# Kernel tuning notes

Measured on AMD Instinct MI355X. Metric: run time of the kernel, lower is better.

## Reference

```python
import jax, jax.numpy as jnp
import numpy as np

ATTRACTION_W = 1.0
REPULSION_W = 1.0
BETA_POS_W = 1.0
BETA_NEG_W = 0.5
K_INST = 256  # max number of distinct instance ids (slice ids)


def setup_inputs() -> dict:
    key = jax.random.key(0)
    B, N, D, K = 4, 65536, 256, K_INST
    k1, k2, k3 = jax.random.split(key, 3)
    beta = jax.random.normal(k1, (B, N, 1), jnp.float32)
    embed = jax.random.normal(k2, (B, N, D), jnp.float32)
    sid = jax.random.randint(k3, (B, N), -1, K)  # -1 = background
    # force exactly one condensation point per instance: hit i (<K) -> sid=i, is_cp
    sid = sid.at[:, :K].set(jnp.broadcast_to(jnp.arange(K), (B, K)))
    is_cp = jnp.zeros((B, N), bool).at[:, :K].set(True)
    return {"beta": beta, "embed": embed, "slice_id": sid, "is_cp": is_cp}


def _loss_single(beta, emb, sid, cp):
    # beta: (N,) logits, emb: (N,D), sid: (N,) int, cp: (N,) bool
    N = sid.shape[0]
    valid = sid >= 0
    cpv = cp & valid  # condensation points with a valid instance id
    # BCE-with-logits: target 1 -> softplus(-x), target 0 -> softplus(x)
    pos = jnp.sum(jnp.where(cpv, jax.nn.softplus(-beta), 0.0)) / jnp.maximum(cpv.sum(), 1)
    noncp = ~cp
    neg = jnp.sum(jnp.where(noncp, jax.nn.softplus(beta), 0.0)) / jnp.maximum(noncp.sum(), 1)
    beta_loss = BETA_POS_W * pos + BETA_NEG_W * neg

    # first CP hit index per instance (segment-min over CP hits), N = "no CP"
    sid_c = jnp.where(valid, sid, 0)
    idx = jnp.arange(N)
    first_cp = jnp.full((K_INST,), N, jnp.int32).at[sid_c].min(
        jnp.where(cpv, idx, N).astype(jnp.int32))
    has_cp = first_cp < N
    cp_emb = emb[jnp.minimum(first_cp, N - 1)]  # (K, D), garbage where no CP

    # attraction: sum over instances of mean ||emb - inst_cp||^2
    d2 = jnp.sum((emb - cp_emb[sid_c]) ** 2, axis=-1)  # (N,)
    w = valid & has_cp[sid_c]
    seg_sum = jnp.zeros((K_INST,), jnp.float32).at[sid_c].add(jnp.where(w, d2, 0.0))
    seg_cnt = jnp.zeros((K_INST,), jnp.float32).at[sid_c].add(w.astype(jnp.float32))
    attraction = jnp.sum(jnp.where(seg_cnt > 0, seg_sum / jnp.maximum(seg_cnt, 1.0), 0.0))
    attraction = attraction * ATTRACTION_W

    # repulsion: mean exp(-||cp_i - cp_j||^2) over all CP pairs (incl. diagonal)
    pd2 = jnp.sum((cp_emb[:, None, :] - cp_emb[None, :, :]) ** 2, axis=-1)  # (K,K)
    pmask = has_cp[:, None] & has_cp[None, :]
    M = has_cp.sum()
    rep = jnp.sum(jnp.where(pmask, jnp.exp(-pd2), 0.0)) / jnp.maximum(M * M, 1)
    rep = jnp.where(M > 1, rep * REPULSION_W, 0.0)

    loss = beta_loss + attraction + rep
    ok = (valid.sum() > 0) & (cpv.sum() > 0)
    return jnp.where(ok, loss, 0.0), ok


def reference(beta, embed, slice_id, is_cp):
    losses, oks = jax.vmap(_loss_single)(beta.squeeze(-1), embed, slice_id, is_cp)
    cnt = oks.sum()
    return jnp.where(cnt > 0, losses.sum() / jnp.maximum(cnt, 1), 0.0)
```

## Files before the change

### kernel.cpp

```cpp
#include <hip/hip_runtime.h>
#include <math.h>

#define K_INST 256
#define ATTRACTION_W 1.0f
#define REPULSION_W 1.0f
#define BETA_POS_W 1.0f
#define BETA_NEG_W 0.5f

__device__ inline float softplusf(float x) {
    return fmaxf(x, 0.f) + log1pf(expf(-fabsf(x)));
}

__device__ inline float waveReduceSumF(float v) {
    for (int o = 32; o; o >>= 1) v += __shfl_xor(v, o);
    return v;
}
__device__ inline int waveReduceSumI(int v) {
    for (int o = 32; o; o >>= 1) v += __shfl_xor(v, o);
    return v;
}

__global__ void init_kernel(int* first_cp, float* seg_sum, int* seg_cnt,
                            float* pos_sum, float* neg_sum, float* rep_sum,
                            int* cpv_cnt, int* noncp_cnt, int* valid_cnt,
                            int N, int B) {
    int idx = blockIdx.x * blockDim.x + threadIdx.x;
    if (idx < B * K_INST) {
        first_cp[idx] = N;
        seg_sum[idx] = 0.f;
        seg_cnt[idx] = 0;
    }
    if (idx < B) {
        pos_sum[idx] = 0.f; neg_sum[idx] = 0.f; rep_sum[idx] = 0.f;
        cpv_cnt[idx] = 0; noncp_cnt[idx] = 0; valid_cnt[idx] = 0;
    }
}

__global__ void stats_kernel(const float* __restrict__ beta,
                             const int* __restrict__ sid,
                             const int* __restrict__ is_cp,
                             int* first_cp,
                             float* pos_sum, float* neg_sum,
                             int* cpv_cnt, int* noncp_cnt, int* valid_cnt,
                             int N) {
    int b = blockIdx.y;
    int base = (blockIdx.x * blockDim.x + threadIdx.x) * 4;
    const float* betaB = beta + (size_t)b * N;
    const int* sidB = sid + (size_t)b * N;
    const int* cpB = is_cp + (size_t)b * N;

    float pos = 0.f, neg = 0.f;
    int c_cpv = 0, c_non = 0, c_val = 0;

    int4 s4 = *(const int4*)(sidB + base);
    int4 c4 = *(const int4*)(cpB + base);
    float4 x4 = *(const float4*)(betaB + base);
    int ss[4] = {s4.x, s4.y, s4.z, s4.w};
    int cc[4] = {c4.x, c4.y, c4.z, c4.w};
    float xx[4] = {x4.x, x4.y, x4.z, x4.w};
    #pragma unroll
    for (int e = 0; e < 4; ++e) {
        bool valid = ss[e] >= 0;
        bool cpv = cc[e] && valid;
        if (cpv) {
            pos += softplusf(-xx[e]);
            c_cpv++;
            atomicMin(&first_cp[b * K_INST + ss[e]], base + e);
        }
        if (!cc[e]) {
            neg += softplusf(xx[e]);
            c_non++;
        }
        c_val += valid ? 1 : 0;
    }

    __shared__ float sf[2][4];
    __shared__ int si[3][4];
    pos = waveReduceSumF(pos);
    neg = waveReduceSumF(neg);
    c_cpv = waveReduceSumI(c_cpv);
    c_non = waveReduceSumI(c_non);
    c_val = waveReduceSumI(c_val);
    int wave = threadIdx.x >> 6, lane = threadIdx.x & 63;
    if (lane == 0) {
        sf[0][wave] = pos; sf[1][wave] = neg;
        si[0][wave] = c_cpv; si[1][wave] = c_non; si[2][wave] = c_val;
    }
    __syncthreads();
    if (threadIdx.x == 0) {
        float p = sf[0][0] + sf[0][1] + sf[0][2] + sf[0][3];
        float n = sf[1][0] + sf[1][1] + sf[1][2] + sf[1][3];
        int a = si[0][0] + si[0][1] + si[0][2] + si[0][3];
        int c = si[1][0] + si[1][1] + si[1][2] + si[1][3];
        int v = si[2][0] + si[2][1] + si[2][2] + si[2][3];
        if (p != 0.f) atomicAdd(&pos_sum[b], p);
        if (n != 0.f) atomicAdd(&neg_sum[b], n);
        if (a) atomicAdd(&cpv_cnt[b], a);
        if (c) atomicAdd(&noncp_cnt[b], c);
        if (v) atomicAdd(&valid_cnt[b], v);
    }
}

__global__ void gather_kernel(const float* __restrict__ embed,
                              const int* __restrict__ first_cp,
                              float* __restrict__ cp_emb,
                              float* __restrict__ cp_embT, int N) {
    int b = blockIdx.y;
    int k0 = blockIdx.x * 64;
    __shared__ float tile[64][257];
    const float* embB = embed + (size_t)b * N * 256;
    const int* fcB = first_cp + b * K_INST;

    int r = threadIdx.x >> 2;
    int q = threadIdx.x & 3;
    int src = fcB[k0 + r];
    if (src >= N) src = N - 1;
    const float4* srow = (const float4*)(embB + (size_t)src * 256);
    float4* drow = (float4*)(cp_emb + ((size_t)b * K_INST + k0 + r) * 256);
    #pragma unroll
    for (int c = 0; c < 16; ++c) {
        float4 v = srow[q * 16 + c];
        drow[q * 16 + c] = v;
        int col = q * 64 + c * 4;
        tile[r][col + 0] = v.x;
        tile[r][col + 1] = v.y;
        tile[r][col + 2] = v.z;
        tile[r][col + 3] = v.w;
    }
    __syncthreads();
    int kk = threadIdx.x & 63;
    int dg = threadIdx.x >> 6;
    float* T = cp_embT + (size_t)b * K_INST * 256;
    #pragma unroll
    for (int dd = 0; dd < 64; ++dd) {
        int d = dg * 64 + dd;
        T[(size_t)d * 256 + k0 + kk] = tile[kk][d];
    }
}

__global__ void attraction_kernel(const float* __restrict__ embed,
                                  const int* __restrict__ sid,
                                  const int* __restrict__ first_cp,
                                  const float* __restrict__ cp_emb,
                                  float* seg_sum, int* seg_cnt,
                                  int N, int blocks_per_batch) {
    int b = blockIdx.y;
    __shared__ float s_sum[K_INST];
    __shared__ int s_cnt[K_INST];
    for (int k = threadIdx.x; k < K_INST; k += blockDim.x) { s_sum[k] = 0.f; s_cnt[k] = 0; }
    __syncthreads();

    int wave = threadIdx.x >> 6;
    int lane = threadIdx.x & 63;
    int waves_per_batch = blocks_per_batch * 4;
    int wid = blockIdx.x * 4 + wave;
    int stride = waves_per_batch * 8;

    const float* embB = embed + (size_t)b * N * 256;
    const float* cpB  = cp_emb + (size_t)b * K_INST * 256;
    const int* sidB   = sid + (size_t)b * N;
    const int* fcB    = first_cp + b * K_INST;

    for (int i = wid * 8; i < N; i += stride) {
        int4 sa = *(const int4*)(sidB + i);
        int4 sb = *(const int4*)(sidB + i + 4);
        int ss[8] = {sa.x, sa.y, sa.z, sa.w, sb.x, sb.y, sb.z, sb.w};

        float4 e[8];
        #pragma unroll
        for (int j = 0; j < 8; ++j)
            e[j] = *(const float4*)(embB + (size_t)(i + j) * 256 + lane * 4);

        float v[8];
        unsigned act = 0;
        #pragma unroll
        for (int j = 0; j < 8; ++j) {
            v[j] = 0.f;
            int s = ss[j];
            if (s >= 0 && fcB[s] < N) {
                act |= (1u << j);
                float4 c = *(const float4*)(cpB + (size_t)s * 256 + lane * 4);
                float d0 = e[j].x - c.x, d1 = e[j].y - c.y;
                float d2 = e[j].z - c.z, d3 = e[j].w - c.w;
                v[j] = d0 * d0 + d1 * d1 + d2 * d2 + d3 * d3;
            }
        }
        #pragma unroll
        for (int j = 0; j < 8; ++j) v[j] = waveReduceSumF(v[j]);
        if (lane == 0) {
            #pragma unroll
            for (int j = 0; j < 8; ++j) {
                if (act & (1u << j)) {
                    atomicAdd(&s_sum[ss[j]], v[j]);
                    atomicAdd(&s_cnt[ss[j]], 1);
                }
            }
        }
    }
    __syncthreads();
    for (int k = threadIdx.x; k < K_INST; k += blockDim.x) {
        if (s_cnt[k]) {
            atomicAdd(&seg_sum[b * K_INST + k], s_sum[k]);
            atomicAdd(&seg_cnt[b * K_INST + k], s_cnt[k]);
        }
    }
}

__global__ void repulsion_kernel(const float* __restrict__ cp_emb,
                                 const float* __restrict__ cp_embT,
                                 const int* __restrict__ first_cp,
                                 float* rep_sum, int N) {
    int b = blockIdx.y;
    int i0 = blockIdx.x * 8;
    __shared__ float srow[8][260];
    const float* cpB = cp_emb + (size_t)b * K_INST * 256;
    const float* T = cp_embT + (size_t)b * K_INST * 256;

    {
        int r = threadIdx.x >> 5, cc = (threadIdx.x & 31) * 8;
        float4 a = *(const float4*)(cpB + (size_t)(i0 + r) * 256 + cc);
        float4 bv = *(const float4*)(cpB + (size_t)(i0 + r) * 256 + cc + 4);
        srow[r][cc + 0] = a.x;  srow[r][cc + 1] = a.y;
        srow[r][cc + 2] = a.z;  srow[r][cc + 3] = a.w;
        srow[r][cc + 4] = bv.x; srow[r][cc + 5] = bv.y;
        srow[r][cc + 6] = bv.z; srow[r][cc + 7] = bv.w;
    }
    __syncthreads();

    int j = threadIdx.x;
    bool has_j = first_cp[b * K_INST + j] < N;
    float acc[8] = {0.f, 0.f, 0.f, 0.f, 0.f, 0.f, 0.f, 0.f};
    for (int d = 0; d < 256; d += 2) {
        float v0 = T[(size_t)d * 256 + j];
        float v1 = T[(size_t)(d + 1) * 256 + j];
        #pragma unroll
        for (int r = 0; r < 8; ++r) {
            float f0 = srow[r][d] - v0;
            float f1 = srow[r][d + 1] - v1;
            acc[r] += f0 * f0 + f1 * f1;
        }
    }
    float val = 0.f;
    #pragma unroll
    for (int r = 0; r < 8; ++r) {
        bool has_i = first_cp[b * K_INST + i0 + r] < N;
        if (has_i && has_j) val += expf(-acc[r]);
    }
    __shared__ float sf[4];
    val = waveReduceSumF(val);
    int wave = threadIdx.x >> 6, lane = threadIdx.x & 63;
    if (lane == 0) sf[wave] = val;
    __syncthreads();
    if (threadIdx.x == 0) {
        atomicAdd(&rep_sum[b], sf[0] + sf[1] + sf[2] + sf[3]);
    }
}

__global__ void final_kernel(const int* __restrict__ first_cp,
                             const float* __restrict__ seg_sum,
                             const int* __restrict__ seg_cnt,
                             const float* __restrict__ pos_sum,
                             const float* __restrict__ neg_sum,
                             const float* __restrict__ rep_sum,
                             const int* __restrict__ cpv_cnt,
                             const int* __restrict__ noncp_cnt,
                             const int* __restrict__ valid_cnt,
                             float* out, int N, int B) {
    __shared__ float s_att[4];
    __shared__ int s_m[4];
    float loss_sum = 0.f;
    int ok_cnt = 0;
    int wave = threadIdx.x >> 6, lane = threadIdx.x & 63;
    for (int b = 0; b < B; ++b) {
        int k = threadIdx.x;
        int fc = first_cp[b * K_INST + k];
        int has = (fc < N) ? 1 : 0;
        int cnt = seg_cnt[b * K_INST + k];
        float att = (cnt > 0) ? (seg_sum[b * K_INST + k] / (float)cnt) : 0.f;
        att = waveReduceSumF(att);
        has = waveReduceSumI(has);
        if (lane == 0) { s_att[wave] = att; s_m[wave] = has; }
        __syncthreads();
        if (threadIdx.x == 0) {
            float attraction = (s_att[0] + s_att[1] + s_att[2] + s_att[3]) * ATTRACTION_W;
            int M = s_m[0] + s_m[1] + s_m[2] + s_m[3];
            float pos = pos_sum[b] / fmaxf((float)cpv_cnt[b], 1.f);
            float neg = neg_sum[b] / fmaxf((float)noncp_cnt[b], 1.f);
            float beta_loss = BETA_POS_W * pos + BETA_NEG_W * neg;
            float rep = 0.f;
            if (M > 1) {
                float mm = (float)M * (float)M;
                rep = (rep_sum[b] / fmaxf(mm, 1.f)) * REPULSION_W;
            }
            float loss = beta_loss + attraction + rep;
            bool ok = (valid_cnt[b] > 0) && (cpv_cnt[b] > 0);
            if (ok) { loss_sum += loss; ok_cnt += 1; }
        }
        __syncthreads();
    }
    if (threadIdx.x == 0) {
        out[0] = (ok_cnt > 0) ? (loss_sum / (float)ok_cnt) : 0.f;
    }
}

extern "C" void kernel_launch(void* const* d_in, const int* in_sizes, int n_in,
                              void* d_out, int out_size, void* d_ws, size_t ws_size,
                              hipStream_t stream) {
    const float* beta  = (const float*)d_in[0];
    const float* embed = (const float*)d_in[1];
    const int* sid     = (const int*)d_in[2];
    const int* is_cp   = (const int*)d_in[3];
    float* out = (float*)d_out;

    const int N = 65536;
    const int B = in_sizes[0] / N;
    (void)n_in; (void)out_size; (void)ws_size;

    char* ws = (char*)d_ws;
    int*   first_cp  = (int*)(ws + 0);
    float* seg_sum   = (float*)(ws + 4096);
    int*   seg_cnt   = (int*)(ws + 8192);
    float* pos_sum   = (float*)(ws + 12288);
    float* neg_sum   = (float*)(ws + 12352);
    float* rep_sum   = (float*)(ws + 12416);
    int*   cpv_cnt   = (int*)(ws + 12480);
    int*   noncp_cnt = (int*)(ws + 12544);
    int*   valid_cnt = (int*)(ws + 12608);
    float* cp_emb    = (float*)(ws + 16384);
    float* cp_embT   = (float*)(ws + 16384 + (size_t)B * K_INST * 256 * 4);

    init_kernel<<<dim3((B * K_INST + 255) / 256), dim3(256), 0, stream>>>(
        first_cp, seg_sum, seg_cnt, pos_sum, neg_sum, rep_sum,
        cpv_cnt, noncp_cnt, valid_cnt, N, B);

    stats_kernel<<<dim3(N / 1024, B), dim3(256), 0, stream>>>(
        beta, sid, is_cp, first_cp, pos_sum, neg_sum,
        cpv_cnt, noncp_cnt, valid_cnt, N);

    gather_kernel<<<dim3(K_INST / 64, B), dim3(256), 0, stream>>>(
        embed, first_cp, cp_emb, cp_embT, N);

    const int blocks_per_batch = 512;
    attraction_kernel<<<dim3(blocks_per_batch, B), dim3(256), 0, stream>>>(
        embed, sid, first_cp, cp_emb, seg_sum, seg_cnt, N, blocks_per_batch);

    repulsion_kernel<<<dim3(K_INST / 8, B), dim3(256), 0, stream>>>(
        cp_emb, cp_embT, first_cp, rep_sum, N);

    final_kernel<<<dim3(1), dim3(256), 0, stream>>>(
        first_cp, seg_sum, seg_cnt, pos_sum, neg_sum, rep_sum,
        cpv_cnt, noncp_cnt, valid_cnt, out, N, B);
}
```

Before: 120.0 us.

## Fuse attraction and repulsion into one launch and simplify stats and gather

Attraction and repulsion now run in a single kernel: the first 32 blocks per batch compute repulsion and the remaining 512 do the attraction pass, so one launch and its serialization gap go away and the small repulsion work overlaps the bandwidth-bound attraction. The attraction loop now issues all centroid loads without branching, clamping invalid ids to row 0, and applies the validity check only at accumulation time, which gives more memory-level parallelism. The stats kernel processes one element per thread instead of four, with four times as many blocks. The gather kernel uses one 64-thread block per instance and writes the transpose directly, without shared memory. These changes trade vectorised loads and coalesced transpose writes for more parallelism and fewer launches.

```diff
diff --git a/kernel.cpp b/kernel.cpp
--- a/kernel.cpp
+++ b/kernel.cpp
@@ -44,34 +44,24 @@
                              int* cpv_cnt, int* noncp_cnt, int* valid_cnt,
                              int N) {
     int b = blockIdx.y;
-    int base = (blockIdx.x * blockDim.x + threadIdx.x) * 4;
-    const float* betaB = beta + (size_t)b * N;
-    const int* sidB = sid + (size_t)b * N;
-    const int* cpB = is_cp + (size_t)b * N;
-
+    int i = blockIdx.x * blockDim.x + threadIdx.x;
+    size_t gi = (size_t)b * N + i;
+    int s = sid[gi];
+    int cp = is_cp[gi];
+    float x = beta[gi];
+
+    bool valid = s >= 0;
+    bool cpv = cp && valid;
     float pos = 0.f, neg = 0.f;
-    int c_cpv = 0, c_non = 0, c_val = 0;
-
-    int4 s4 = *(const int4*)(sidB + base);
-    int4 c4 = *(const int4*)(cpB + base);
-    float4 x4 = *(const float4*)(betaB + base);
-    int ss[4] = {s4.x, s4.y, s4.z, s4.w};
-    int cc[4] = {c4.x, c4.y, c4.z, c4.w};
-    float xx[4] = {x4.x, x4.y, x4.z, x4.w};
-    #pragma unroll
-    for (int e = 0; e < 4; ++e) {
-        bool valid = ss[e] >= 0;
-        bool cpv = cc[e] && valid;
-        if (cpv) {
-            pos += softplusf(-xx[e]);
-            c_cpv++;
-            atomicMin(&first_cp[b * K_INST + ss[e]], base + e);
-        }
-        if (!cc[e]) {
-            neg += softplusf(xx[e]);
-            c_non++;
-        }
-        c_val += valid ? 1 : 0;
+    int c_cpv = 0, c_non = 0, c_val = valid ? 1 : 0;
+    if (cpv) {
+        pos = softplusf(-x);
+        c_cpv = 1;
+        atomicMin(&first_cp[b * K_INST + s], i);
+    }
+    if (!cp) {
+        neg = softplusf(x);
+        c_non = 1;
     }
 
     __shared__ float sf[2][4];
@@ -106,153 +96,133 @@
                               float* __restrict__ cp_emb,
                               float* __restrict__ cp_embT, int N) {
     int b = blockIdx.y;
-    int k0 = blockIdx.x * 64;
-    __shared__ float tile[64][257];
+    int k = blockIdx.x;
+    int src = first_cp[b * K_INST + k];
+    if (src >= N) src = N - 1;
+    int lane = threadIdx.x;
     const float* embB = embed + (size_t)b * N * 256;
-    const int* fcB = first_cp + b * K_INST;
-
-    int r = threadIdx.x >> 2;
-    int q = threadIdx.x & 3;
-    int src = fcB[k0 + r];
-    if (src >= N) src = N - 1;
-    const float4* srow = (const float4*)(embB + (size_t)src * 256);
-    float4* drow = (float4*)(cp_emb + ((size_t)b * K_INST + k0 + r) * 256);
-    #pragma unroll
-    for (int c = 0; c < 16; ++c) {
-        float4 v = srow[q * 16 + c];
-        drow[q * 16 + c] = v;
-        int col = q * 64 + c * 4;
-        tile[r][col + 0] = v.x;
-        tile[r][col + 1] = v.y;
-        tile[r][col + 2] = v.z;
-        tile[r][col + 3] = v.w;
-    }
-    __syncthreads();
-    int kk = threadIdx.x & 63;
-    int dg = threadIdx.x >> 6;
+    float4 v = ((const float4*)(embB + (size_t)src * 256))[lane];
+    ((float4*)(cp_emb + ((size_t)b * K_INST + k) * 256))[lane] = v;
     float* T = cp_embT + (size_t)b * K_INST * 256;
-    #pragma unroll
-    for (int dd = 0; dd < 64; ++dd) {
-        int d = dg * 64 + dd;
-        T[(size_t)d * 256 + k0 + kk] = tile[kk][d];
-    }
-}
-
-__global__ void attraction_kernel(const float* __restrict__ embed,
-                                  const int* __restrict__ sid,
-                                  const int* __restrict__ first_cp,
-                                  const float* __restrict__ cp_emb,
-                                  float* seg_sum, int* seg_cnt,
-                                  int N, int blocks_per_batch) {
+    int d = lane * 4;
+    T[(size_t)(d + 0) * 256 + k] = v.x;
+    T[(size_t)(d + 1) * 256 + k] = v.y;
+    T[(size_t)(d + 2) * 256 + k] = v.z;
+    T[(size_t)(d + 3) * 256 + k] = v.w;
+}
+
+__global__ void attraction_repulsion_kernel(
+        const float* __restrict__ embed,
+        const int* __restrict__ sid,
+        const int* __restrict__ first_cp,
+        const float* __restrict__ cp_emb,
+        const float* __restrict__ cp_embT,
+        float* seg_sum, int* seg_cnt, float* rep_sum,
+        int N, int atr_blocks) {
     int b = blockIdx.y;
     __shared__ float s_sum[K_INST];
     __shared__ int s_cnt[K_INST];
-    for (int k = threadIdx.x; k < K_INST; k += blockDim.x) { s_sum[k] = 0.f; s_cnt[k] = 0; }
-    __syncthreads();
-
-    int wave = threadIdx.x >> 6;
-    int lane = threadIdx.x & 63;
-    int waves_per_batch = blocks_per_batch * 4;
-    int wid = blockIdx.x * 4 + wave;
-    int stride = waves_per_batch * 8;
-
-    const float* embB = embed + (size_t)b * N * 256;
-    const float* cpB  = cp_emb + (size_t)b * K_INST * 256;
-    const int* sidB   = sid + (size_t)b * N;
-    const int* fcB    = first_cp + b * K_INST;
-
-    for (int i = wid * 8; i < N; i += stride) {
-        int4 sa = *(const int4*)(sidB + i);
-        int4 sb = *(const int4*)(sidB + i + 4);
-        int ss[8] = {sa.x, sa.y, sa.z, sa.w, sb.x, sb.y, sb.z, sb.w};
-
-        float4 e[8];
-        #pragma unroll
-        for (int j = 0; j < 8; ++j)
-            e[j] = *(const float4*)(embB + (size_t)(i + j) * 256 + lane * 4);
-
-        float v[8];
-        unsigned act = 0;
-        #pragma unroll
-        for (int j = 0; j < 8; ++j) {
-            v[j] = 0.f;
-            int s = ss[j];
-            if (s >= 0 && fcB[s] < N) {
-                act |= (1u << j);
-                float4 c = *(const float4*)(cpB + (size_t)s * 256 + lane * 4);
-                float d0 = e[j].x - c.x, d1 = e[j].y - c.y;
-                float d2 = e[j].z - c.z, d3 = e[j].w - c.w;
-                v[j] = d0 * d0 + d1 * d1 + d2 * d2 + d3 * d3;
-            }
-        }
-        #pragma unroll
-        for (int j = 0; j < 8; ++j) v[j] = waveReduceSumF(v[j]);
-        if (lane == 0) {
-            #pragma unroll
-            for (int j = 0; j < 8; ++j) {
-                if (act & (1u << j)) {
-                    atomicAdd(&s_sum[ss[j]], v[j]);
-                    atomicAdd(&s_cnt[ss[j]], 1);
-                }
-            }
-        }
-    }
-    __syncthreads();
-    for (int k = threadIdx.x; k < K_INST; k += blockDim.x) {
-        if (s_cnt[k]) {
-            atomicAdd(&seg_sum[b * K_INST + k], s_sum[k]);
-            atomicAdd(&seg_cnt[b * K_INST + k], s_cnt[k]);
-        }
-    }
-}
-
-__global__ void repulsion_kernel(const float* __restrict__ cp_emb,
-                                 const float* __restrict__ cp_embT,
-                                 const int* __restrict__ first_cp,
-                                 float* rep_sum, int N) {
-    int b = blockIdx.y;
-    int i0 = blockIdx.x * 8;
     __shared__ float srow[8][260];
+    __shared__ float sf[4];
+
     const float* cpB = cp_emb + (size_t)b * K_INST * 256;
-    const float* T = cp_embT + (size_t)b * K_INST * 256;
-
-    {
-        int r = threadIdx.x >> 5, cc = (threadIdx.x & 31) * 8;
-        float4 a = *(const float4*)(cpB + (size_t)(i0 + r) * 256 + cc);
-        float4 bv = *(const float4*)(cpB + (size_t)(i0 + r) * 256 + cc + 4);
-        srow[r][cc + 0] = a.x;  srow[r][cc + 1] = a.y;
-        srow[r][cc + 2] = a.z;  srow[r][cc + 3] = a.w;
-        srow[r][cc + 4] = bv.x; srow[r][cc + 5] = bv.y;
-        srow[r][cc + 6] = bv.z; srow[r][cc + 7] = bv.w;
-    }
-    __syncthreads();
-
-    int j = threadIdx.x;
-    bool has_j = first_cp[b * K_INST + j] < N;
-    float acc[8] = {0.f, 0.f, 0.f, 0.f, 0.f, 0.f, 0.f, 0.f};
-    for (int d = 0; d < 256; d += 2) {
-        float v0 = T[(size_t)d * 256 + j];
-        float v1 = T[(size_t)(d + 1) * 256 + j];
+    const int* fcB = first_cp + b * K_INST;
+
+    if (blockIdx.x < 32) {
+        int i0 = blockIdx.x * 8;
+        const float* T = cp_embT + (size_t)b * K_INST * 256;
+        {
+            int r = threadIdx.x >> 5, cc = (threadIdx.x & 31) * 8;
+            float4 a = *(const float4*)(cpB + (size_t)(i0 + r) * 256 + cc);
+            float4 bv = *(const float4*)(cpB + (size_t)(i0 + r) * 256 + cc + 4);
+            srow[r][cc + 0] = a.x;  srow[r][cc + 1] = a.y;
+            srow[r][cc + 2] = a.z;  srow[r][cc + 3] = a.w;
+            srow[r][cc + 4] = bv.x; srow[r][cc + 5] = bv.y;
+            srow[r][cc + 6] = bv.z; srow[r][cc + 7] = bv.w;
+        }
+        __syncthreads();
+
+        int j = threadIdx.x;
+        bool has_j = fcB[j] < N;
+        float acc[8] = {0.f, 0.f, 0.f, 0.f, 0.f, 0.f, 0.f, 0.f};
+        for (int d = 0; d < 256; d += 2) {
+            float v0 = T[(size_t)d * 256 + j];
+            float v1 = T[(size_t)(d + 1) * 256 + j];
+            #pragma unroll
+            for (int r = 0; r < 8; ++r) {
+                float f0 = srow[r][d] - v0;
+                float f1 = srow[r][d + 1] - v1;
+                acc[r] += f0 * f0 + f1 * f1;
+            }
+        }
+        float val = 0.f;
         #pragma unroll
         for (int r = 0; r < 8; ++r) {
-            float f0 = srow[r][d] - v0;
-            float f1 = srow[r][d + 1] - v1;
-            acc[r] += f0 * f0 + f1 * f1;
-        }
-    }
-    float val = 0.f;
-    #pragma unroll
-    for (int r = 0; r < 8; ++r) {
-        bool has_i = first_cp[b * K_INST + i0 + r] < N;
-        if (has_i && has_j) val += expf(-acc[r]);
-    }
-    __shared__ float sf[4];
-    val = waveReduceSumF(val);
-    int wave = threadIdx.x >> 6, lane = threadIdx.x & 63;
-    if (lane == 0) sf[wave] = val;
-    __syncthreads();
-    if (threadIdx.x == 0) {
-        atomicAdd(&rep_sum[b], sf[0] + sf[1] + sf[2] + sf[3]);
+            bool has_i = fcB[i0 + r] < N;
+            if (has_i && has_j) val += expf(-acc[r]);
+        }
+        val = waveReduceSumF(val);
+        int wave = threadIdx.x >> 6, lane = threadIdx.x & 63;
+        if (lane == 0) sf[wave] = val;
+        __syncthreads();
+        if (threadIdx.x == 0)
+            atomicAdd(&rep_sum[b], sf[0] + sf[1] + sf[2] + sf[3]);
+    } else {
+        for (int k = threadIdx.x; k < K_INST; k += blockDim.x) { s_sum[k] = 0.f; s_cnt[k] = 0; }
+        __syncthreads();
+
+        int bx = blockIdx.x - 32;
+        int wave = threadIdx.x >> 6;
+        int lane = threadIdx.x & 63;
+        int waves_per_batch = atr_blocks * 4;
+        int wid = bx * 4 + wave;
+        int stride = waves_per_batch * 8;
+
+        const float* embB = embed + (size_t)b * N * 256;
+        const int* sidB = sid + (size_t)b * N;
+
+        for (int i = wid * 8; i < N; i += stride) {
+            int4 sa = *(const int4*)(sidB + i);
+            int4 sb = *(const int4*)(sidB + i + 4);
+            int ss[8] = {sa.x, sa.y, sa.z, sa.w, sb.x, sb.y, sb.z, sb.w};
+
+            float4 e[8], c[8];
+            #pragma unroll
+            for (int j = 0; j < 8; ++j)
+                e[j] = *(const float4*)(embB + (size_t)(i + j) * 256 + lane * 4);
+            #pragma unroll
+            for (int j = 0; j < 8; ++j) {
+                int sc = ss[j] < 0 ? 0 : ss[j];
+                c[j] = *(const float4*)(cpB + (size_t)sc * 256 + lane * 4);
+            }
+
+            float v[8];
+            #pragma unroll
+            for (int j = 0; j < 8; ++j) {
+                float d0 = e[j].x - c[j].x, d1 = e[j].y - c[j].y;
+                float d2 = e[j].z - c[j].z, d3 = e[j].w - c[j].w;
+                v[j] = d0 * d0 + d1 * d1 + d2 * d2 + d3 * d3;
+            }
+            #pragma unroll
+            for (int j = 0; j < 8; ++j) v[j] = waveReduceSumF(v[j]);
+            if (lane == 0) {
+                #pragma unroll
+                for (int j = 0; j < 8; ++j) {
+                    int s = ss[j];
+                    if (s >= 0 && fcB[s] < N) {
+                        atomicAdd(&s_sum[s], v[j]);
+                        atomicAdd(&s_cnt[s], 1);
+                    }
+                }
+            }
+        }
+        __syncthreads();
+        for (int k = threadIdx.x; k < K_INST; k += blockDim.x) {
+            if (s_cnt[k]) {
+                atomicAdd(&seg_sum[b * K_INST + k], s_sum[k]);
+                atomicAdd(&seg_cnt[b * K_INST + k], s_cnt[k]);
+            }
+        }
     }
 }
 
@@ -333,19 +303,17 @@
         first_cp, seg_sum, seg_cnt, pos_sum, neg_sum, rep_sum,
         cpv_cnt, noncp_cnt, valid_cnt, N, B);
 
-    stats_kernel<<<dim3(N / 1024, B), dim3(256), 0, stream>>>(
+    stats_kernel<<<dim3(N / 256, B), dim3(256), 0, stream>>>(
         beta, sid, is_cp, first_cp, pos_sum, neg_sum,
         cpv_cnt, noncp_cnt, valid_cnt, N);
 
-    gather_kernel<<<dim3(K_INST / 64, B), dim3(256), 0, stream>>>(
+    gather_kernel<<<dim3(K_INST, B), dim3(64), 0, stream>>>(
         embed, first_cp, cp_emb, cp_embT, N);
 
-    const int blocks_per_batch = 512;
-    attraction_kernel<<<dim3(blocks_per_batch, B), dim3(256), 0, stream>>>(
-        embed, sid, first_cp, cp_emb, seg_sum, seg_cnt, N, blocks_per_batch);
-
-    repulsion_kernel<<<dim3(K_INST / 8, B), dim3(256), 0, stream>>>(
-        cp_emb, cp_embT, first_cp, rep_sum, N);
+    const int atr_blocks = 512;
+    attraction_repulsion_kernel<<<dim3(32 + atr_blocks, B), dim3(256), 0, stream>>>(
+        embed, sid, first_cp, cp_emb, cp_embT,
+        seg_sum, seg_cnt, rep_sum, N, atr_blocks);
 
     final_kernel<<<dim3(1), dim3(256), 0, stream>>>(
         first_cp, seg_sum, seg_cnt, pos_sum, neg_sum, rep_sum,
```

After: 103.1 us. -14.1%, faster.
